# Performance work log

Measured on AMD Instinct MI355X. Metric: run time of the kernel, lower is better.

Reference implementation:

```python
import jax, jax.numpy as jnp
import numpy as np

RHO = 0.1

def setup_inputs() -> dict:
    key = jax.random.key(0)
    k1, k2 = jax.random.split(key)
    B, C, H, W = 64, 256, 56, 56
    features = jax.random.normal(k1, (B, C, H, W), dtype=jnp.float32)
    grad = jax.random.normal(k2, (B, C, H, W), dtype=jnp.float32)
    return {"features": features, "grad": grad}


def reference(features, grad):
    # attribution = relu(grad * features), elementwise
    attribution = jax.nn.relu(grad * features)
    B = attribution.shape[0]
    flat_attr = attribution.reshape(B, -1)          # [B, C*H*W]
    k = int(RHO * flat_attr.shape[1])               # static: 80281
    topk_val, _ = jax.lax.top_k(flat_attr, k)       # [B, k], descending
    threshold = topk_val[:, -1].reshape(-1, 1, 1, 1)  # k-th largest per sample
    mask = (attribution <= threshold).astype(features.dtype)
    return features * mask
```

## Files before the change

### kernel.cpp

```cpp
#include <hip/hip_runtime.h>

namespace {
constexpr int NS   = 64;
constexpr int NPS  = 802816;
constexpr int NPSV = NPS / 4;
constexpr unsigned KSEL = 80281u;
constexpr unsigned SENT = 0xFFFFFFFFu;
constexpr int NB   = 8192;
constexpr int GX   = 32;
constexpr int SEGV = NPSV / GX;
constexpr int SEG  = NPS / GX;
constexpr int PAIRCAP = 1024;
constexpr int CAP_LDS = 20480;
constexpr int BRB  = 8;
constexpr int CHUNKS = 128;
constexpr int CH_STRIDE = NPSV / CHUNKS;
constexpr unsigned RU_RANK = 12129u;
constexpr unsigned RL_RANK = 14086u;
constexpr int GXA  = 64;
constexpr int SEGCAP2 = 20736;
constexpr int TAILF4  = 1056;
typedef float f32x4 __attribute__((ext_vector_type(4)));
}

__device__ __forceinline__ void nt_store4(float4* dst, const float4& v) {
    f32x4 w; w.x = v.x; w.y = v.y; w.z = v.z; w.w = v.w;
    __builtin_nontemporal_store(w, reinterpret_cast<f32x4*>(dst));
}

template <int NBINS>
__device__ void select_in_lds(const unsigned* __restrict__ h, unsigned K,
                              unsigned* bin, unsigned* rem) {
    constexpr int BPT = NBINS / 256;
    __shared__ unsigned cs[256];
    __shared__ unsigned fB, fR;
    const int t = threadIdx.x;
    unsigned s = 0;
    for (int j = 0; j < BPT; ++j) s += h[t * BPT + j];
    cs[t] = s;
    if (t == 0) { fB = SENT; fR = 0u; }
    __syncthreads();
    unsigned suf = 0;
    for (int j = t + 1; j < 256; ++j) suf += cs[j];
    if (suf < K && suf + s >= K) {
        unsigned cur = suf;
        for (int j = BPT - 1; j >= 0; --j) {
            const unsigned c = h[t * BPT + j];
            if (cur < K && cur + c >= K) { fB = (unsigned)(t * BPT + j); fR = K - cur; break; }
            cur += c;
        }
    }
    __syncthreads();
    const unsigned rb = fB, rr = fR;
    __syncthreads();
    *bin = rb; *rem = rr;
}

__global__ __launch_bounds__(256) void bracket_kernel(const float4* __restrict__ f,
                                                      const float4* __restrict__ g,
                                                      unsigned short* __restrict__ bh,
                                                      unsigned* __restrict__ fail) {
    __shared__ unsigned h[NB];
    const int jb = blockIdx.x, b = blockIdx.y, t = threadIdx.x;
    if (jb == 0 && b == 0 && t == 0) fail[0] = 0u;
    for (int k = t; k < NB; k += 256) h[k] = 0u;
    __syncthreads();
    const size_t base = (size_t)b * NPSV;
#define HBIN(p) { if ((p) > 0.0f) atomicAdd(&h[__float_as_uint(p) >> 18], 1u); }
    for (int c = 0; c < CHUNKS / BRB; c += 2) {
        const int ch = jb * (CHUNKS / BRB) + c;
        const size_t i0 = base + (size_t)ch * CH_STRIDE + t;
        const size_t i1 = base + (size_t)(ch + 1) * CH_STRIDE + t;
        const float4 fa = f[i0], fb = f[i1];
        const float4 ga = g[i0], gb = g[i1];
        HBIN(fa.x * ga.x) HBIN(fa.y * ga.y) HBIN(fa.z * ga.z) HBIN(fa.w * ga.w)
        HBIN(fb.x * gb.x) HBIN(fb.y * gb.y) HBIN(fb.z * gb.z) HBIN(fb.w * gb.w)
    }
#undef HBIN
    __syncthreads();
    unsigned short* o = bh + (size_t)(b * BRB + jb) * NB;
    for (int k = t; k < NB; k += 256) o[k] = (unsigned short)h[k];
}

__global__ __launch_bounds__(256) void bracket_scan_kernel(const unsigned short* __restrict__ bh,
                                                           unsigned* __restrict__ binLU) {
    __shared__ unsigned h[NB];
    const int b = blockIdx.x, t = threadIdx.x;
    for (int k = t; k < NB; k += 256) {
        unsigned s = 0;
        const unsigned short* p = bh + (size_t)b * BRB * NB + k;
        for (int j = 0; j < BRB; ++j) s += p[(size_t)j * NB];
        h[k] = s;
    }
    __syncthreads();
    unsigned bU, rU, bL, rL;
    select_in_lds<NB>(h, RU_RANK, &bU, &rU);
    select_in_lds<NB>(h, RL_RANK, &bL, &rL);
    if (t == 0) {
        binLU[2 * b]     = (bL == SENT) ? 0u : bL;
        binLU[2 * b + 1] = (bU == SENT) ? (unsigned)(NB - 1) : bU;
    }
}

__global__ __launch_bounds__(256) void scatter0_kernel(const float4* __restrict__ f,
                                                       const float4* __restrict__ g,
                                                       float4* __restrict__ out,
                                                       unsigned* __restrict__ pv,
                                                       unsigned* __restrict__ ppos,
                                                       const unsigned* __restrict__ binLU,
                                                       unsigned* __restrict__ cnts,
                                                       unsigned* __restrict__ chis,
                                                       unsigned* __restrict__ fail) {
    const int j = blockIdx.x, b = blockIdx.y, t = threadIdx.x;
    const unsigned binL = binLU[2 * b], binU = binLU[2 * b + 1];
    __shared__ unsigned cnt;
    __shared__ unsigned wsum[4];
    __shared__ unsigned lv[PAIRCAP];
    __shared__ unsigned lp[PAIRCAP];
    if (t == 0) cnt = 0u;
    __syncthreads();
    const size_t base = (size_t)b * NPSV + (size_t)j * SEGV;
    unsigned chi = 0;
#define PROC(FC, GC, IDX, CIDX, OC) { \
        const float p_ = (FC) * (GC); \
        const unsigned u_ = __float_as_uint(p_); \
        const unsigned pre_ = u_ >> 18; \
        const bool pos_ = p_ > 0.0f; \
        const bool drop_ = pos_ && (pre_ > binU); \
        OC = drop_ ? 0.0f : (FC); \
        chi += drop_; \
        if (pos_ && pre_ >= binL && pre_ <= binU) { \
            const unsigned x_ = atomicAdd(&cnt, 1u); \
            if (x_ < PAIRCAP) { lv[x_] = u_; lp[x_] = (unsigned)((IDX) * 4) + CIDX; } \
        } }
#define PROC4(FV, GV, IDX, OV) \
        PROC(FV.x, GV.x, IDX, 0u, OV.x) PROC(FV.y, GV.y, IDX, 1u, OV.y) \
        PROC(FV.z, GV.z, IDX, 2u, OV.z) PROC(FV.w, GV.w, IDX, 3u, OV.w)

    constexpr int ITERS = SEGV / 256;
    constexpr int TAIL0 = ITERS * 256;
    float4 cf = f[base + t], cg = g[base + t];
    for (int it = 0; it < ITERS; ++it) {
        const int i = it * 256 + t;
        float4 nf, ng;
        if (it < ITERS - 1) { nf = f[base + i + 256]; ng = g[base + i + 256]; }
        else if (t < SEGV - TAIL0) { nf = f[base + TAIL0 + t]; ng = g[base + TAIL0 + t]; }
        float4 o;
        PROC4(cf, cg, j * SEGV + i, o)
        nt_store4(&out[base + i], o);
        cf = nf; cg = ng;
    }
    if (t < SEGV - TAIL0) {
        float4 o;
        PROC4(cf, cg, j * SEGV + TAIL0 + t, o)
        nt_store4(&out[base + TAIL0 + t], o);
    }
#undef PROC4
#undef PROC
    for (int off = 32; off; off >>= 1) chi += __shfl_down(chi, off);
    if ((t & 63) == 0) wsum[t >> 6] = chi;
    __syncthreads();
    const unsigned ctot = cnt;
    const unsigned c = (ctot > PAIRCAP) ? PAIRCAP : ctot;
    const size_t segp = (size_t)(b * GX + j) * PAIRCAP;
    for (unsigned k = t; k < c; k += 256) { pv[segp + k] = lv[k]; ppos[segp + k] = lp[k]; }
    if (t == 0) {
        chis[b * GX + j] = wsum[0] + wsum[1] + wsum[2] + wsum[3];
        cnts[b * GX + j] = c;
        if (ctot > PAIRCAP) fail[0] = 1u;
    }
}

__global__ __launch_bounds__(256) void select0_kernel(const unsigned* __restrict__ pv,
                                                      const unsigned* __restrict__ ppos,
                                                      const unsigned* __restrict__ binLU,
                                                      const unsigned* __restrict__ cnts,
                                                      const unsigned* __restrict__ chis,
                                                      unsigned* __restrict__ fail,
                                                      float* __restrict__ thrF,
                                                      float* __restrict__ out) {
    if (fail[0]) return;
    const int b = blockIdx.x, t = threadIdx.x;
    __shared__ unsigned vals[CAP_LDS];
    __shared__ unsigned hist[NB];
    __shared__ unsigned soff[GX + 1];
    __shared__ unsigned sh_chi;
    __shared__ float sh_thr;
    if (t == 0) {
        unsigned o = 0;
        for (int j = 0; j < GX; ++j) { soff[j] = o; o += cnts[b * GX + j]; }
        soff[GX] = o;
        unsigned c = 0;
        for (int j = 0; j < GX; ++j) c += chis[b * GX + j];
        sh_chi = c;
    }
    __syncthreads();
    const unsigned ncand = soff[GX];
    const unsigned chi = sh_chi;
    if (chi >= KSEL) { if (t == 0) fail[0] = 1u; return; }
    if (ncand > CAP_LDS) { if (t == 0) fail[0] = 1u; return; }
    const unsigned Krem = KSEL - chi;
    bool zeroThr = false;
    if (Krem > ncand) {
        if (binLU[2 * b] == 0u) zeroThr = true;
        else { if (t == 0) fail[0] = 1u; return; }
    }
    for (int j = 0; j < GX; ++j) {
        const unsigned c = soff[j + 1] - soff[j];
        const unsigned* s = pv + (size_t)(b * GX + j) * PAIRCAP;
        for (unsigned i = t; i < c; i += 256) vals[soff[j] + i] = s[i];
    }
    if (zeroThr) {
        if (t == 0) { sh_thr = 0.0f; thrF[b] = 0.0f; }
        __syncthreads();
    } else {
        for (int k = t; k < NB; k += 256) hist[k] = 0u;
        __syncthreads();
        for (unsigned i = t; i < ncand; i += 256) atomicAdd(&hist[vals[i] >> 18], 1u);
        __syncthreads();
        unsigned P1, r1; select_in_lds<NB>(hist, Krem, &P1, &r1);
        __syncthreads();
        for (int k = t; k < NB; k += 256) hist[k] = 0u;
        __syncthreads();
        for (unsigned i = t; i < ncand; i += 256) {
            const unsigned u = vals[i];
            if ((u >> 18) == P1) atomicAdd(&hist[(u >> 5) & (NB - 1u)], 1u);
        }
        __syncthreads();
        unsigned P2, r2; select_in_lds<NB>(hist, r1, &P2, &r2);
        __syncthreads();
        if (t < 32) hist[t] = 0u;
        __syncthreads();
        const unsigned pref = (P1 << 13) | P2;
        for (unsigned i = t; i < ncand; i += 256) {
            const unsigned u = vals[i];
            if ((u >> 5) == pref) atomicAdd(&hist[u & 31u], 1u);
        }
        __syncthreads();
        if (t == 0) {
            unsigned cur = 0, b3 = 0;
            for (int q = 31; q >= 0; --q) {
                const unsigned c = hist[q];
                if (cur < r2 && cur + c >= r2) { b3 = (unsigned)q; break; }
                cur += c;
            }
            const float thr = __uint_as_float((P1 << 18) | (P2 << 5) | b3);
            sh_thr = thr; thrF[b] = thr;
        }
        __syncthreads();
    }
    const float thr = sh_thr;
    float* ob = out + (size_t)b * NPS;
    for (int j = 0; j < GX; ++j) {
        const unsigned c = soff[j + 1] - soff[j];
        const unsigned* qp = ppos + (size_t)(b * GX + j) * PAIRCAP;
        const unsigned so = soff[j];
        for (unsigned i = t; i < c; i += 256) {
            if (__uint_as_float(vals[so + i]) > thr) ob[qp[i]] = 0.0f;
        }
    }
}

__global__ __launch_bounds__(256) void scatter_fb_kernel(const float4* __restrict__ f,
                                                         const float4* __restrict__ g,
                                                         unsigned* __restrict__ list,
                                                         unsigned* __restrict__ cnts,
                                                         unsigned* __restrict__ chis,
                                                         const unsigned* __restrict__ fail,
                                                         int mode, int segCap) {
    if (mode == 1 && fail[0] == 0u) return;
    const int j = blockIdx.x, b = blockIdx.y, t = threadIdx.x;
    __shared__ unsigned cnt;
    if (t == 0) cnt = 0u;
    __syncthreads();
    unsigned* __restrict__ seg = list + (size_t)b * NPS + (size_t)j * SEG;
    const size_t base = (size_t)b * NPSV + (size_t)j * SEGV;
    for (int i = t; i < SEGV; i += 256) {
        const float4 fv = f[base + i];
        const float4 gv = g[base + i];
        const float p0 = fv.x * gv.x, p1 = fv.y * gv.y, p2 = fv.z * gv.z, p3 = fv.w * gv.w;
#define PROCF(p) { if ((p) > 0.0f) { const unsigned x = atomicAdd(&cnt, 1u); \
                   if ((int)x < segCap) seg[x] = __float_as_uint(p); } }
        PROCF(p0) PROCF(p1) PROCF(p2) PROCF(p3)
#undef PROCF
    }
    __syncthreads();
    if (t == 0) {
        cnts[b * GX + j] = (cnt > (unsigned)segCap) ? (unsigned)segCap : cnt;
        chis[b * GX + j] = 0u;
    }
}

__global__ __launch_bounds__(256) void select_fb_kernel(const unsigned* __restrict__ list,
                                                        const unsigned* __restrict__ cnts,
                                                        unsigned* __restrict__ fail,
                                                        float* __restrict__ thrF,
                                                        int mode) {
    if (mode == 1 && fail[0] == 0u) return;
    const int b = blockIdx.x, t = threadIdx.x;
    __shared__ unsigned h[NB];
    __shared__ unsigned segc[GX];
    if (t < GX) segc[t] = cnts[b * GX + t];
    __syncthreads();
    unsigned ncand = 0;
    for (int j = 0; j < GX; ++j) ncand += segc[j];
    if (KSEL > ncand) {
        if (t == 0) thrF[b] = 0.0f;
        return;
    }
    const unsigned* __restrict__ seg0 = list + (size_t)b * NPS;
    for (int k = t; k < NB; k += 256) h[k] = 0u;
    __syncthreads();
    for (int j = 0; j < GX; ++j) {
        const unsigned c = segc[j];
        const unsigned* s = seg0 + (size_t)j * SEG;
        for (unsigned i = t; i < c; i += 256) atomicAdd(&h[s[i] >> 18], 1u);
    }
    __syncthreads();
    unsigned P1, r1; select_in_lds<NB>(h, KSEL, &P1, &r1);
    __syncthreads();
    for (int k = t; k < NB; k += 256) h[k] = 0u;
    __syncthreads();
    for (int j = 0; j < GX; ++j) {
        const unsigned c = segc[j];
        const unsigned* s = seg0 + (size_t)j * SEG;
        for (unsigned i = t; i < c; i += 256) {
            const unsigned u = s[i];
            if ((u >> 18) == P1) atomicAdd(&h[(u >> 5) & (NB - 1u)], 1u);
        }
    }
    __syncthreads();
    unsigned P2, r2; select_in_lds<NB>(h, r1, &P2, &r2);
    __syncthreads();
    if (t < 32) h[t] = 0u;
    __syncthreads();
    const unsigned pref = (P1 << 13) | P2;
    for (int j = 0; j < GX; ++j) {
        const unsigned c = segc[j];
        const unsigned* s = seg0 + (size_t)j * SEG;
        for (unsigned i = t; i < c; i += 256) {
            const unsigned u = s[i];
            if ((u >> 5) == pref) atomicAdd(&h[u & 31u], 1u);
        }
    }
    __syncthreads();
    if (t == 0) {
        unsigned cur = 0, b3 = 0;
        for (int q = 31; q >= 0; --q) {
            const unsigned c = h[q];
            if (cur < r2 && cur + c >= r2) { b3 = (unsigned)q; break; }
            cur += c;
        }
        thrF[b] = __uint_as_float((P1 << 18) | (P2 << 5) | b3);
    }
}

__global__ __launch_bounds__(256) void apply_fb_kernel(const float4* __restrict__ f,
                                                       const float4* __restrict__ g,
                                                       const float* __restrict__ thrF,
                                                       float4* __restrict__ out,
                                                       const unsigned* __restrict__ fail,
                                                       int mode, int tailCut) {
    if (mode == 1 && fail[0] == 0u) return;
    const int b = blockIdx.y;
    const float thr = thrF[b];
    const size_t base = (size_t)b * NPSV;
    const int limit = NPSV - ((b == NS - 1) ? tailCut : 0);
    const int stride = gridDim.x * blockDim.x;
    for (int i = blockIdx.x * 256 + threadIdx.x; i < limit; i += stride) {
        const float4 fv = f[base + i];
        const float4 gv = g[base + i];
        float4 o;
        o.x = (fv.x * gv.x > thr) ? 0.0f : fv.x;
        o.y = (fv.y * gv.y > thr) ? 0.0f : fv.y;
        o.z = (fv.z * gv.z > thr) ? 0.0f : fv.z;
        o.w = (fv.w * gv.w > thr) ? 0.0f : fv.w;
        out[base + i] = o;
    }
}

__global__ void apply_tail_kernel(const float4* __restrict__ f, const float4* __restrict__ g,
                                  const float* __restrict__ thrF,
                                  float4* __restrict__ out, int tailCut) {
    const float thr = thrF[NS - 1];
    asm volatile("" :: "v"(thr));
    __syncthreads();
    const size_t base = (size_t)NS * NPSV - tailCut;
    for (int i = threadIdx.x; i < tailCut; i += 256) {
        const float4 fv = f[base + i];
        const float4 gv = g[base + i];
        float4 o;
        o.x = (fv.x * gv.x > thr) ? 0.0f : fv.x;
        o.y = (fv.y * gv.y > thr) ? 0.0f : fv.y;
        o.z = (fv.z * gv.z > thr) ? 0.0f : fv.z;
        o.w = (fv.w * gv.w > thr) ? 0.0f : fv.w;
        out[base + i] = o;
    }
}

extern "C" void kernel_launch(void* const* d_in, const int* in_sizes, int n_in,
                              void* d_out, int out_size, void* d_ws, size_t ws_size,
                              hipStream_t stream) {
    const float* f = (const float*)d_in[0];
    const float* g = (const float*)d_in[1];
    float* out = (float*)d_out;

    const size_t pairU32  = (size_t)NS * GX * PAIRCAP;
    const size_t brBytes  = (size_t)NS * BRB * NB * sizeof(unsigned short);
    const size_t bigBytes = (pairU32 * 8 > brBytes) ? pairU32 * 8 : brBytes;
    const size_t smallU32 = 2 * NS + NS * GX + NS * GX + 1 + NS;
    const size_t need     = bigBytes + smallU32 * 4;

    if (ws_size >= need) {
        char* w = (char*)d_ws;
        unsigned short* bh = (unsigned short*)w;
        unsigned* pv   = (unsigned*)w;
        unsigned* ppos = pv + pairU32;
        unsigned* sm   = (unsigned*)(w + bigBytes);
        unsigned* binLU = sm;
        unsigned* cnts  = binLU + 2 * NS;
        unsigned* chis  = cnts + NS * GX;
        unsigned* fail  = chis + NS * GX;
        float*    thrF  = (float*)(fail + 1);

        bracket_kernel<<<dim3(BRB, NS), 256, 0, stream>>>((const float4*)f, (const float4*)g,
                                                          bh, fail);
        bracket_scan_kernel<<<NS, 256, 0, stream>>>(bh, binLU);
        scatter0_kernel<<<dim3(GX, NS), 256, 0, stream>>>((const float4*)f, (const float4*)g,
                                                          (float4*)out, pv, ppos, binLU,
                                                          cnts, chis, fail);
        select0_kernel<<<NS, 256, 0, stream>>>(pv, ppos, binLU, cnts, chis, fail, thrF, out);
        scatter_fb_kernel<<<dim3(GX, NS), 256, 0, stream>>>((const float4*)f, (const float4*)g,
                                                            (unsigned*)out, cnts, chis, fail,
                                                            1, SEG);
        select_fb_kernel<<<NS, 256, 0, stream>>>((const unsigned*)out, cnts, fail, thrF, 1);
        apply_fb_kernel<<<dim3(GXA, NS), 256, 0, stream>>>((const float4*)f, (const float4*)g,
                                                           thrF, (float4*)out, fail, 1, 0);
    } else {
        unsigned* list = (unsigned*)out;
        unsigned* sm   = (unsigned*)out + ((size_t)NS * NPS - 4 * TAILF4);
        unsigned* cnts = sm;
        unsigned* chis = cnts + NS * GX;
        unsigned* fail = chis + NS * GX;
        float*    thrF = (float*)(fail + 1);

        scatter_fb_kernel<<<dim3(GX, NS), 256, 0, stream>>>((const float4*)f, (const float4*)g,
                                                            list, cnts, chis, fail, 2, SEGCAP2);
        select_fb_kernel<<<NS, 256, 0, stream>>>(list, cnts, fail, thrF, 2);
        apply_fb_kernel<<<dim3(GXA, NS), 256, 0, stream>>>((const float4*)f, (const float4*)g,
                                                           thrF, (float4*)out, fail, 2, TAILF4);
        apply_tail_kernel<<<1, 256, 0, stream>>>((const float4*)f, (const float4*)g,
                                                 thrF, (float4*)out, TAILF4);
    }
}
```

Measured before the change: 230.0 us.

## Stream scatter0 inputs through per-wave LDS ring via global_load_lds

Replaces the register double-buffered load loop in scatter0 with a 5-slot per-wave LDS ring filled by direct global-to-LDS loads, keeping four iterations of f and g in flight and pacing them with explicit vmcnt waits. This aims to hide global memory latency on the streaming pass. It also drops the nontemporal output stores in favour of plain stores, adds 40KB of LDS per block (which may reduce occupancy), and relies on hand-written waitcnt counts that must match the instruction ordering the compiler emits.

Result: slower. 279.8 us (+21.7%).

```diff
diff --git a/kernel.cpp b/kernel.cpp
--- a/kernel.cpp
+++ b/kernel.cpp
@@ -20,12 +20,14 @@
 constexpr int GXA  = 64;
 constexpr int SEGCAP2 = 20736;
 constexpr int TAILF4  = 1056;
-typedef float f32x4 __attribute__((ext_vector_type(4)));
-}
-
-__device__ __forceinline__ void nt_store4(float4* dst, const float4& v) {
-    f32x4 w; w.x = v.x; w.y = v.y; w.z = v.z; w.w = v.w;
-    __builtin_nontemporal_store(w, reinterpret_cast<f32x4*>(dst));
+constexpr int NBUF = 5;
+constexpr int KITER = 24;
+}
+
+__device__ __forceinline__ void gload_lds16(const float4* gsrc, float4* ldst) {
+    __builtin_amdgcn_global_load_lds(
+        (const __attribute__((address_space(1))) unsigned int*)gsrc,
+        (__attribute__((address_space(3))) unsigned int*)ldst, 16, 0, 0);
 }
 
 template <int NBINS>
@@ -112,7 +114,10 @@
                                                        unsigned* __restrict__ chis,
                                                        unsigned* __restrict__ fail) {
     const int j = blockIdx.x, b = blockIdx.y, t = threadIdx.x;
+    const int wid = t >> 6, lane = t & 63;
     const unsigned binL = binLU[2 * b], binU = binLU[2 * b + 1];
+    __shared__ float4 ldsF[4][NBUF][64];
+    __shared__ float4 ldsG[4][NBUF][64];
     __shared__ unsigned cnt;
     __shared__ unsigned wsum[4];
     __shared__ unsigned lv[PAIRCAP];
@@ -137,24 +142,50 @@
         PROC(FV.x, GV.x, IDX, 0u, OV.x) PROC(FV.y, GV.y, IDX, 1u, OV.y) \
         PROC(FV.z, GV.z, IDX, 2u, OV.z) PROC(FV.w, GV.w, IDX, 3u, OV.w)
 
-    constexpr int ITERS = SEGV / 256;
-    constexpr int TAIL0 = ITERS * 256;
-    float4 cf = f[base + t], cg = g[base + t];
-    for (int it = 0; it < ITERS; ++it) {
-        const int i = it * 256 + t;
-        float4 nf, ng;
-        if (it < ITERS - 1) { nf = f[base + i + 256]; ng = g[base + i + 256]; }
-        else if (t < SEGV - TAIL0) { nf = f[base + TAIL0 + t]; ng = g[base + TAIL0 + t]; }
-        float4 o;
-        PROC4(cf, cg, j * SEGV + i, o)
-        nt_store4(&out[base + i], o);
-        cf = nf; cg = ng;
-    }
-    if (t < SEGV - TAIL0) {
-        float4 o;
-        PROC4(cf, cg, j * SEGV + TAIL0 + t, o)
-        nt_store4(&out[base + TAIL0 + t], o);
-    }
+#define BODY(K, PREFETCH) { \
+        const int slot_ = (K) % NBUF; \
+        const float4 fv = ldsF[wid][slot_][lane]; \
+        const float4 gv = ldsG[wid][slot_][lane]; \
+        if (PREFETCH) { \
+            const int kp_ = (K) + 4, sp_ = kp_ % NBUF; \
+            gload_lds16(&f[base + kp_ * 256 + t], &ldsF[wid][sp_][0]); \
+            gload_lds16(&g[base + kp_ * 256 + t], &ldsG[wid][sp_][0]); \
+        } \
+        float4 o; \
+        PROC4(fv, gv, j * SEGV + (K) * 256 + t, o) \
+        out[base + (K) * 256 + t] = o; }
+
+#pragma unroll
+    for (int k = 0; k < 4; ++k) {
+        gload_lds16(&f[base + k * 256 + t], &ldsF[wid][k][0]);
+        gload_lds16(&g[base + k * 256 + t], &ldsG[wid][k][0]);
+    }
+    for (int k = 0; k < 4; ++k) {
+        asm volatile("s_waitcnt vmcnt(6)" ::: "memory");
+        __builtin_amdgcn_sched_barrier(0);
+        BODY(k, 1)
+    }
+    for (int k = 4; k < KITER - 4; ++k) {
+        asm volatile("s_waitcnt vmcnt(10)" ::: "memory");
+        __builtin_amdgcn_sched_barrier(0);
+        BODY(k, 1)
+    }
+    asm volatile("s_waitcnt vmcnt(0)" ::: "memory");
+    __builtin_amdgcn_sched_barrier(0);
+    for (int k = KITER - 4; k < KITER; ++k) {
+        BODY(k, 0)
+    }
+    {
+        if (t < SEGV - KITER * 256) {
+            const int i = KITER * 256 + t;
+            const float4 fv = f[base + i];
+            const float4 gv = g[base + i];
+            float4 o;
+            PROC4(fv, gv, j * SEGV + i, o)
+            out[base + i] = o;
+        }
+    }
+#undef BODY
 #undef PROC4
 #undef PROC
     for (int off = 32; off; off >>= 1) chi += __shfl_down(chi, off);
```

## Interleave scatter0 tiles across fewer, larger blocks with bigger pair capacity

Applied to the files above, without the earlier changes.

scatter0 now launches half as many blocks per sample. Each block walks 49 interleaved 256-float4 tiles strided by the grid width instead of one contiguous segment, and the explicit register double-buffering is dropped. Per-block pair capacity doubles to match the larger share of elements. The fallback kernels keep the old 32-way split under new constants. This trades launch count and per-block setup against lower occupancy and the loss of manual prefetch. It also assumes select0 and its count arrays stay consistent with the new grid width, which is not visible here.

After: 219.8 us. 1.05x faster.

```diff
diff --git a/kernel.cpp b/kernel.cpp
--- a/kernel.cpp
+++ b/kernel.cpp
@@ -7,16 +7,18 @@
 constexpr unsigned KSEL = 80281u;
 constexpr unsigned SENT = 0xFFFFFFFFu;
 constexpr int NB   = 8192;
-constexpr int GX   = 32;
-constexpr int SEGV = NPSV / GX;
-constexpr int SEG  = NPS / GX;
-constexpr int PAIRCAP = 1024;
+constexpr int GX   = 16;
+constexpr int TPB  = 49;
+constexpr int PAIRCAP = 2048;
 constexpr int CAP_LDS = 20480;
 constexpr int BRB  = 8;
 constexpr int CHUNKS = 128;
 constexpr int CH_STRIDE = NPSV / CHUNKS;
 constexpr unsigned RU_RANK = 12129u;
 constexpr unsigned RL_RANK = 14086u;
+constexpr int GXF  = 32;
+constexpr int SEGVF = NPSV / GXF;
+constexpr int SEGF  = NPS / GXF;
 constexpr int GXA  = 64;
 constexpr int SEGCAP2 = 20736;
 constexpr int TAILF4  = 1056;
@@ -119,7 +121,7 @@
     __shared__ unsigned lp[PAIRCAP];
     if (t == 0) cnt = 0u;
     __syncthreads();
-    const size_t base = (size_t)b * NPSV + (size_t)j * SEGV;
+    const size_t sbase = (size_t)b * NPSV;
     unsigned chi = 0;
 #define PROC(FC, GC, IDX, CIDX, OC) { \
         const float p_ = (FC) * (GC); \
@@ -137,23 +139,13 @@
         PROC(FV.x, GV.x, IDX, 0u, OV.x) PROC(FV.y, GV.y, IDX, 1u, OV.y) \
         PROC(FV.z, GV.z, IDX, 2u, OV.z) PROC(FV.w, GV.w, IDX, 3u, OV.w)
 
-    constexpr int ITERS = SEGV / 256;
-    constexpr int TAIL0 = ITERS * 256;
-    float4 cf = f[base + t], cg = g[base + t];
-    for (int it = 0; it < ITERS; ++it) {
-        const int i = it * 256 + t;
-        float4 nf, ng;
-        if (it < ITERS - 1) { nf = f[base + i + 256]; ng = g[base + i + 256]; }
-        else if (t < SEGV - TAIL0) { nf = f[base + TAIL0 + t]; ng = g[base + TAIL0 + t]; }
+    for (int k = 0; k < TPB; ++k) {
+        const int i = (k * GX + j) * 256 + t;
+        const float4 fv = f[sbase + i];
+        const float4 gv = g[sbase + i];
         float4 o;
-        PROC4(cf, cg, j * SEGV + i, o)
-        nt_store4(&out[base + i], o);
-        cf = nf; cg = ng;
-    }
-    if (t < SEGV - TAIL0) {
-        float4 o;
-        PROC4(cf, cg, j * SEGV + TAIL0 + t, o)
-        nt_store4(&out[base + TAIL0 + t], o);
+        PROC4(fv, gv, i, o)
+        nt_store4(&out[sbase + i], o);
     }
 #undef PROC4
 #undef PROC
@@ -273,9 +265,9 @@
     __shared__ unsigned cnt;
     if (t == 0) cnt = 0u;
     __syncthreads();
-    unsigned* __restrict__ seg = list + (size_t)b * NPS + (size_t)j * SEG;
-    const size_t base = (size_t)b * NPSV + (size_t)j * SEGV;
-    for (int i = t; i < SEGV; i += 256) {
+    unsigned* __restrict__ seg = list + (size_t)b * NPS + (size_t)j * SEGF;
+    const size_t base = (size_t)b * NPSV + (size_t)j * SEGVF;
+    for (int i = t; i < SEGVF; i += 256) {
         const float4 fv = f[base + i];
         const float4 gv = g[base + i];
         const float p0 = fv.x * gv.x, p1 = fv.y * gv.y, p2 = fv.z * gv.z, p3 = fv.w * gv.w;
@@ -286,8 +278,8 @@
     }
     __syncthreads();
     if (t == 0) {
-        cnts[b * GX + j] = (cnt > (unsigned)segCap) ? (unsigned)segCap : cnt;
-        chis[b * GX + j] = 0u;
+        cnts[b * GXF + j] = (cnt > (unsigned)segCap) ? (unsigned)segCap : cnt;
+        chis[b * GXF + j] = 0u;
     }
 }
 
@@ -299,11 +291,11 @@
     if (mode == 1 && fail[0] == 0u) return;
     const int b = blockIdx.x, t = threadIdx.x;
     __shared__ unsigned h[NB];
-    __shared__ unsigned segc[GX];
-    if (t < GX) segc[t] = cnts[b * GX + t];
+    __shared__ unsigned segc[GXF];
+    if (t < GXF) segc[t] = cnts[b * GXF + t];
     __syncthreads();
     unsigned ncand = 0;
-    for (int j = 0; j < GX; ++j) ncand += segc[j];
+    for (int j = 0; j < GXF; ++j) ncand += segc[j];
     if (KSEL > ncand) {
         if (t == 0) thrF[b] = 0.0f;
         return;
@@ -311,9 +303,9 @@
     const unsigned* __restrict__ seg0 = list + (size_t)b * NPS;
     for (int k = t; k < NB; k += 256) h[k] = 0u;
     __syncthreads();
-    for (int j = 0; j < GX; ++j) {
+    for (int j = 0; j < GXF; ++j) {
         const unsigned c = segc[j];
-        const unsigned* s = seg0 + (size_t)j * SEG;
+        const unsigned* s = seg0 + (size_t)j * SEGF;
         for (unsigned i = t; i < c; i += 256) atomicAdd(&h[s[i] >> 18], 1u);
     }
     __syncthreads();
@@ -321,9 +313,9 @@
     __syncthreads();
     for (int k = t; k < NB; k += 256) h[k] = 0u;
     __syncthreads();
-    for (int j = 0; j < GX; ++j) {
+    for (int j = 0; j < GXF; ++j) {
         const unsigned c = segc[j];
-        const unsigned* s = seg0 + (size_t)j * SEG;
+        const unsigned* s = seg0 + (size_t)j * SEGF;
         for (unsigned i = t; i < c; i += 256) {
             const unsigned u = s[i];
             if ((u >> 18) == P1) atomicAdd(&h[(u >> 5) & (NB - 1u)], 1u);
@@ -335,9 +327,9 @@
     if (t < 32) h[t] = 0u;
     __syncthreads();
     const unsigned pref = (P1 << 13) | P2;
-    for (int j = 0; j < GX; ++j) {
+    for (int j = 0; j < GXF; ++j) {
         const unsigned c = segc[j];
-        const unsigned* s = seg0 + (size_t)j * SEG;
+        const unsigned* s = seg0 + (size_t)j * SEGF;
         for (unsigned i = t; i < c; i += 256) {
             const unsigned u = s[i];
             if ((u >> 5) == pref) atomicAdd(&h[u & 31u], 1u);
@@ -408,7 +400,7 @@
     const size_t pairU32  = (size_t)NS * GX * PAIRCAP;
     const size_t brBytes  = (size_t)NS * BRB * NB * sizeof(unsigned short);
     const size_t bigBytes = (pairU32 * 8 > brBytes) ? pairU32 * 8 : brBytes;
-    const size_t smallU32 = 2 * NS + NS * GX + NS * GX + 1 + NS;
+    const size_t smallU32 = 2 * NS + NS * GXF + NS * GXF + 1 + NS;
     const size_t need     = bigBytes + smallU32 * 4;
 
     if (ws_size >= need) {
@@ -419,8 +411,8 @@
         unsigned* sm   = (unsigned*)(w + bigBytes);
         unsigned* binLU = sm;
         unsigned* cnts  = binLU + 2 * NS;
-        unsigned* chis  = cnts + NS * GX;
-        unsigned* fail  = chis + NS * GX;
+        unsigned* chis  = cnts + NS * GXF;
+        unsigned* fail  = chis + NS * GXF;
         float*    thrF  = (float*)(fail + 1);
 
         bracket_kernel<<<dim3(BRB, NS), 256, 0, stream>>>((const float4*)f, (const float4*)g,
@@ -430,9 +422,9 @@
                                                           (float4*)out, pv, ppos, binLU,
                                                           cnts, chis, fail);
         select0_kernel<<<NS, 256, 0, stream>>>(pv, ppos, binLU, cnts, chis, fail, thrF, out);
-        scatter_fb_kernel<<<dim3(GX, NS), 256, 0, stream>>>((const float4*)f, (const float4*)g,
-                                                            (unsigned*)out, cnts, chis, fail,
-                                                            1, SEG);
+        scatter_fb_kernel<<<dim3(GXF, NS), 256, 0, stream>>>((const float4*)f, (const float4*)g,
+                                                             (unsigned*)out, cnts, chis, fail,
+                                                             1, SEGF);
         select_fb_kernel<<<NS, 256, 0, stream>>>((const unsigned*)out, cnts, fail, thrF, 1);
         apply_fb_kernel<<<dim3(GXA, NS), 256, 0, stream>>>((const float4*)f, (const float4*)g,
                                                            thrF, (float4*)out, fail, 1, 0);
@@ -440,12 +432,12 @@
         unsigned* list = (unsigned*)out;
         unsigned* sm   = (unsigned*)out + ((size_t)NS * NPS - 4 * TAILF4);
         unsigned* cnts = sm;
-        unsigned* chis = cnts + NS * GX;
-        unsigned* fail = chis + NS * GX;
+        unsigned* chis = cnts + NS * GXF;
+        unsigned* fail = chis + NS * GXF;
         float*    thrF = (float*)(fail + 1);
 
-        scatter_fb_kernel<<<dim3(GX, NS), 256, 0, stream>>>((const float4*)f, (const float4*)g,
-                                                            list, cnts, chis, fail, 2, SEGCAP2);
+        scatter_fb_kernel<<<dim3(GXF, NS), 256, 0, stream>>>((const float4*)f, (const float4*)g,
+                                                             list, cnts, chis, fail, 2, SEGCAP2);
         select_fb_kernel<<<NS, 256, 0, stream>>>(list, cnts, fail, thrF, 2);
         apply_fb_kernel<<<dim3(GXA, NS), 256, 0, stream>>>((const float4*)f, (const float4*)g,
                                                            thrF, (float4*)out, fail, 2, TAILF4);
```
